# Kernel optimization log

Measured on AMD Instinct MI355X. Metric: run time of the kernel, lower is better.

Reference implementation:

```python
import jax, jax.numpy as jnp
import numpy as np

NCE_T = 0.07   # opt.nce_T
EPS = 1e-8     # torch CosineSimilarity eps
DIAG_FILL = -10.0

N, D = 8192, 256

def setup_inputs() -> dict:
    key = jax.random.key(0)
    kq, kk = jax.random.split(key)
    feat_q = jax.random.normal(kq, (N, D), dtype=jnp.float32)
    feat_k = jax.random.normal(kk, (N, D), dtype=jnp.float32)
    return {"feat_q": feat_q, "feat_k": feat_k}

def reference(feat_q, feat_k):
    # feat_k is detached in the original
    feat_k = jax.lax.stop_gradient(feat_k)
    nq = jnp.linalg.norm(feat_q, axis=-1)            # [N]
    nk = jnp.linalg.norm(feat_k, axis=-1)            # [N]
    # positive cosine similarity (paired rows)
    l_pos = jnp.sum(feat_q * feat_k, axis=-1) / jnp.maximum(nq * nk, EPS)  # [N]
    # full N x N cosine similarity via GEMM (torch does a broadcasted version)
    sim = (feat_q @ feat_k.T) / jnp.maximum(nq[:, None] * nk[None, :], EPS)  # [N,N]
    # mask self-similarities with -10.0 BEFORE dividing by temperature
    diag = jnp.eye(sim.shape[0], dtype=bool)
    l_neg = jnp.where(diag, DIAG_FILL, sim)
    out = jnp.concatenate([l_pos[:, None], l_neg], axis=1) / NCE_T  # [N, N+1]
    # cross-entropy vs target class 0, reduction='none'
    loss = jax.scipy.special.logsumexp(out, axis=1) - out[:, 0]     # [N]
    return loss
```

## Files before the change

### kernel.cpp

```cpp
#include <hip/hip_runtime.h>
#include <stdint.h>
#include <math.h>

#define NROWS 8192
#define DDIM  256
#define BM    128
#define GJ    8
#define COLS_PER_GROUP (NROWS / GJ)

constexpr float INV_T  = 1.0f / 0.07f;
constexpr float LOG2E  = 1.44269504f;
constexpr float K1     = INV_T * LOG2E;

typedef __bf16 bf16x8 __attribute__((ext_vector_type(8)));
typedef float  f32x4  __attribute__((ext_vector_type(4)));

__device__ __forceinline__ void async_copy16(const uint16_t* g, uint16_t* l) {
    __builtin_amdgcn_global_load_lds(
        (const __attribute__((address_space(1))) uint32_t*)g,
        (__attribute__((address_space(3))) uint32_t*)l, 16, 0, 0);
}

__device__ inline uint16_t f2bf(float f) {
    uint32_t u = __float_as_uint(f);
    u += 0x7fffu + ((u >> 16) & 1u);
    return (uint16_t)(u >> 16);
}

__global__ __launch_bounds__(256) void norm_lpos_kernel(
    const float* __restrict__ fq, const float* __restrict__ fk,
    uint16_t* __restrict__ qb, uint16_t* __restrict__ kb,
    float* __restrict__ lpT)
{
    const int wave = threadIdx.x >> 6;
    const int lane = threadIdx.x & 63;
    const int row  = blockIdx.x * 4 + wave;

    float4 vq = ((const float4*)(fq + (size_t)row * DDIM))[lane];
    float4 vk = ((const float4*)(fk + (size_t)row * DDIM))[lane];
    float sq = vq.x*vq.x + vq.y*vq.y + vq.z*vq.z + vq.w*vq.w;
    float sk = vk.x*vk.x + vk.y*vk.y + vk.z*vk.z + vk.w*vk.w;
    float dp = vq.x*vk.x + vq.y*vk.y + vq.z*vk.z + vq.w*vk.w;
    #pragma unroll
    for (int m = 1; m < 64; m <<= 1) {
        sq += __shfl_xor(sq, m, 64);
        sk += __shfl_xor(sk, m, 64);
        dp += __shfl_xor(dp, m, 64);
    }
    float rq = rsqrtf(sq), rk = rsqrtf(sk);

    ushort4 oq, ok;
    oq.x = f2bf(vq.x * rq); oq.y = f2bf(vq.y * rq); oq.z = f2bf(vq.z * rq); oq.w = f2bf(vq.w * rq);
    ok.x = f2bf(vk.x * rk); ok.y = f2bf(vk.y * rk); ok.z = f2bf(vk.z * rk); ok.w = f2bf(vk.w * rk);
    ((ushort4*)(qb + (size_t)row * DDIM))[lane] = oq;
    ((ushort4*)(kb + (size_t)row * DDIM))[lane] = ok;
    if (lane == 0) lpT[row] = dp * rq * rk * INV_T;
}

__global__ __launch_bounds__(256, 2) void nce_main_kernel(
    const uint16_t* __restrict__ qb, const uint16_t* __restrict__ kb,
    float* __restrict__ gpl)
{
    __shared__ __align__(16) uint16_t lds[2 * 128 * 128];

    const int tid    = threadIdx.x;
    const int wave   = tid >> 6;
    const int lane   = tid & 63;
    const int quad   = lane >> 4;
    const int lanelo = lane & 15;
    const int wr     = wave >> 1;
    const int wc     = wave & 1;
    const int rowBase      = blockIdx.x * BM;
    const int colGroupBase = blockIdx.y * COLS_PER_GROUP;

    #pragma unroll
    for (int i = 0; i < 16; ++i) {
        int S   = (wave * 16 + i) * 64 + lane;
        int row = S >> 5;
        int ch  = (S & 31) ^ (row & 31);
        async_copy16(qb + (size_t)(rowBase + row) * DDIM + ch * 8,
                     lds + (size_t)(wave * 16 + i) * 512);
    }
    __syncthreads();

    bf16x8 aq[4][8];
    #pragma unroll
    for (int mt = 0; mt < 4; ++mt) {
        int rq  = wr * 64 + mt * 16 + lanelo;
        int r31 = rq & 31;
        #pragma unroll
        for (int kk = 0; kk < 8; ++kk)
            aq[mt][kk] = *(const bf16x8*)&lds[rq * 256 + (((kk << 2) + quad) ^ r31) * 8];
    }
    __syncthreads();

    int koff[8];
    #pragma unroll
    for (int i = 0; i < 8; ++i) {
        int S   = i * 256 + tid;
        int row = S >> 4;
        int ch  = (S & 15) ^ (row & 15);
        koff[i] = (colGroupBase + row) * DDIM + ch * 8;
    }

    #pragma unroll
    for (int i = 0; i < 8; ++i)
        async_copy16(kb + koff[i], lds + (i * 256 + wave * 64) * 8);
    __syncthreads();

    int bvrow[4];
    #pragma unroll
    for (int nt = 0; nt < 4; ++nt) bvrow[nt] = (wc * 64 + nt * 16 + lanelo) * 128;

    float l_run[16];
    #pragma unroll
    for (int i = 0; i < 16; ++i) l_run[i] = 0.f;

    for (int jt = 0; jt < 8; ++jt) {
        f32x4 acc[4][4];
        #pragma unroll
        for (int mt = 0; mt < 4; ++mt)
            #pragma unroll
            for (int nt = 0; nt < 4; ++nt)
                acc[mt][nt] = (f32x4){0.f, 0.f, 0.f, 0.f};

        #pragma unroll
        for (int h = 0; h < 2; ++h) {
            const int p    = jt * 2 + h;
            const int buf  = p & 1;
            const int boff = buf << 14;

            if (p < 15) {
                const int np  = p + 1;
                const int soff = ((np >> 1) << 15) + ((np & 1) << 7);
                const int doff = (buf ^ 1) << 14;
                #pragma unroll
                for (int i = 0; i < 8; ++i)
                    async_copy16(kb + koff[i] + soff,
                                 lds + doff + (i * 256 + wave * 64) * 8);
            }

            #pragma unroll
            for (int kc = 0; kc < 4; ++kc) {
                bf16x8 bv[4];
                #pragma unroll
                for (int nt = 0; nt < 4; ++nt)
                    bv[nt] = *(const bf16x8*)&lds[boff + bvrow[nt] + (((kc << 2) + quad) ^ lanelo) * 8];
                #pragma unroll
                for (int mt = 0; mt < 4; ++mt)
                    #pragma unroll
                    for (int nt = 0; nt < 4; ++nt)
                        acc[mt][nt] = __builtin_amdgcn_mfma_f32_16x16x32_bf16(
                            aq[mt][h * 4 + kc], bv[nt], acc[mt][nt], 0, 0, 0);
            }
            __syncthreads();
        }

        #pragma unroll
        for (int mt = 0; mt < 4; ++mt)
            #pragma unroll
            for (int rg = 0; rg < 4; ++rg) {
                float s = 0.f;
                #pragma unroll
                for (int nt = 0; nt < 4; ++nt)
                    s += exp2f(fmaf(acc[mt][nt][rg], K1, -K1));
                l_run[mt * 4 + rg] += s;
            }
    }

    #pragma unroll
    for (int i = 0; i < 16; ++i) {
        float v = l_run[i];
        v += __shfl_xor(v, 1, 64);
        v += __shfl_xor(v, 2, 64);
        v += __shfl_xor(v, 4, 64);
        v += __shfl_xor(v, 8, 64);
        l_run[i] = v;
    }
    float* pl = (float*)lds;
    if (lanelo == 0) {
        #pragma unroll
        for (int mt = 0; mt < 4; ++mt)
            #pragma unroll
            for (int rg = 0; rg < 4; ++rg) {
                int lr = wr * 64 + mt * 16 + quad * 4 + rg;
                pl[wc * 128 + lr] = l_run[mt * 4 + rg];
            }
    }
    __syncthreads();
    if (tid < 128) {
        float L = pl[tid] + pl[128 + tid];
        gpl[(size_t)blockIdx.y * NROWS + rowBase + tid] = L;
    }
}

__global__ __launch_bounds__(256) void finalize_kernel(
    const float* __restrict__ gpl, const float* __restrict__ lpT,
    float* __restrict__ out)
{
    int t = blockIdx.x * 256 + threadIdx.x;
    if (t >= NROWS) return;
    float L = 0.f;
    #pragma unroll
    for (int g = 0; g < GJ; ++g) L += gpl[g * NROWS + t];
    out[t] = INV_T + __logf(L) - lpT[t];
}

extern "C" void kernel_launch(void* const* d_in, const int* in_sizes, int n_in,
                              void* d_out, int out_size, void* d_ws, size_t ws_size,
                              hipStream_t stream) {
    const float* fq = (const float*)d_in[0];
    const float* fk = (const float*)d_in[1];
    char* ws = (char*)d_ws;
    uint16_t* qb  = (uint16_t*)(ws);
    uint16_t* kb  = (uint16_t*)(ws + 4194304);
    float*    lpT = (float*)(ws + 8388608);
    float*    gpl = (float*)(ws + 8421376);

    norm_lpos_kernel<<<NROWS / 4, 256, 0, stream>>>(fq, fk, qb, kb, lpT);
    dim3 grid(NROWS / BM, GJ);
    nce_main_kernel<<<grid, 256, 0, stream>>>(qb, kb, gpl);
    finalize_kernel<<<NROWS / 256, 256, 0, stream>>>(gpl, lpT, (float*)d_out);
}
```

Measured before the change: 113.7 us.

## Stream Q and K tiles in 32-wide K-chunks instead of caching Q in registers

```diff
diff --git a/kernel.cpp b/kernel.cpp
--- a/kernel.cpp
+++ b/kernel.cpp
@@ -5,7 +5,8 @@
 #define NROWS 8192
 #define DDIM  256
 #define BM    128
-#define GJ    8
+#define BN    128
+#define GJ    16
 #define COLS_PER_GROUP (NROWS / GJ)
 
 constexpr float INV_T  = 1.0f / 0.07f;
@@ -57,11 +58,11 @@
     if (lane == 0) lpT[row] = dp * rq * rk * INV_T;
 }
 
-__global__ __launch_bounds__(256, 2) void nce_main_kernel(
+__global__ __launch_bounds__(256) void nce_main_kernel(
     const uint16_t* __restrict__ qb, const uint16_t* __restrict__ kb,
     float* __restrict__ gpl)
 {
-    __shared__ __align__(16) uint16_t lds[2 * 128 * 128];
+    __shared__ __align__(16) uint16_t lds[2][2][128 * 32];
 
     const int tid    = threadIdx.x;
     const int wave   = tid >> 6;
@@ -73,50 +74,40 @@
     const int rowBase      = blockIdx.x * BM;
     const int colGroupBase = blockIdx.y * COLS_PER_GROUP;
 
-    #pragma unroll
-    for (int i = 0; i < 16; ++i) {
-        int S   = (wave * 16 + i) * 64 + lane;
-        int row = S >> 5;
-        int ch  = (S & 31) ^ (row & 31);
-        async_copy16(qb + (size_t)(rowBase + row) * DDIM + ch * 8,
-                     lds + (size_t)(wave * 16 + i) * 512);
+    const uint16_t* qsrc[2];
+    const uint16_t* ksrc[2];
+    int dstoff[2];
+    #pragma unroll
+    for (int i = 0; i < 2; ++i) {
+        int S   = i * 256 + tid;
+        int row = S >> 2, cp = S & 3;
+        int cg  = ((cp + (row >> 2)) & 3) ^ (row & 3);
+        qsrc[i] = qb + (size_t)(rowBase + row) * DDIM + cg * 8;
+        ksrc[i] = kb + (size_t)(colGroupBase + row) * DDIM + cg * 8;
+        dstoff[i] = (i * 256 + wave * 64) * 8;
+    }
+
+    int avoff[4], bvoff[4];
+    #pragma unroll
+    for (int t = 0; t < 4; ++t) {
+        int ra = wr * 64 + t * 16 + lanelo;
+        avoff[t] = ra * 32 + ((((quad ^ (ra & 3)) - (ra >> 2)) & 3) * 8);
+        int rb = wc * 64 + t * 16 + lanelo;
+        bvoff[t] = rb * 32 + ((((quad ^ (rb & 3)) - (rb >> 2)) & 3) * 8);
+    }
+
+    #pragma unroll
+    for (int i = 0; i < 2; ++i) {
+        async_copy16(qsrc[i], &lds[0][0][0] + dstoff[i]);
+        async_copy16(ksrc[i], &lds[0][1][0] + dstoff[i]);
     }
     __syncthreads();
 
-    bf16x8 aq[4][8];
-    #pragma unroll
-    for (int mt = 0; mt < 4; ++mt) {
-        int rq  = wr * 64 + mt * 16 + lanelo;
-        int r31 = rq & 31;
-        #pragma unroll
-        for (int kk = 0; kk < 8; ++kk)
-            aq[mt][kk] = *(const bf16x8*)&lds[rq * 256 + (((kk << 2) + quad) ^ r31) * 8];
-    }
-    __syncthreads();
-
-    int koff[8];
-    #pragma unroll
-    for (int i = 0; i < 8; ++i) {
-        int S   = i * 256 + tid;
-        int row = S >> 4;
-        int ch  = (S & 15) ^ (row & 15);
-        koff[i] = (colGroupBase + row) * DDIM + ch * 8;
-    }
-
-    #pragma unroll
-    for (int i = 0; i < 8; ++i)
-        async_copy16(kb + koff[i], lds + (i * 256 + wave * 64) * 8);
-    __syncthreads();
-
-    int bvrow[4];
-    #pragma unroll
-    for (int nt = 0; nt < 4; ++nt) bvrow[nt] = (wc * 64 + nt * 16 + lanelo) * 128;
-
     float l_run[16];
     #pragma unroll
     for (int i = 0; i < 16; ++i) l_run[i] = 0.f;
 
-    for (int jt = 0; jt < 8; ++jt) {
+    for (int jt = 0; jt < COLS_PER_GROUP / BN; ++jt) {
         f32x4 acc[4][4];
         #pragma unroll
         for (int mt = 0; mt < 4; ++mt)
@@ -125,34 +116,34 @@
                 acc[mt][nt] = (f32x4){0.f, 0.f, 0.f, 0.f};
 
         #pragma unroll
-        for (int h = 0; h < 2; ++h) {
-            const int p    = jt * 2 + h;
-            const int buf  = p & 1;
-            const int boff = buf << 14;
-
-            if (p < 15) {
-                const int np  = p + 1;
-                const int soff = ((np >> 1) << 15) + ((np & 1) << 7);
-                const int doff = (buf ^ 1) << 14;
+        for (int kk = 0; kk < 8; ++kk) {
+            const int p   = jt * 8 + kk;
+            const int buf = p & 1;
+
+            if (p < 31) {
+                const int np = p + 1;
+                const int qo = (np & 7) << 5;
+                const int ko = ((np >> 3) << 15) + ((np & 7) << 5);
                 #pragma unroll
-                for (int i = 0; i < 8; ++i)
-                    async_copy16(kb + koff[i] + soff,
-                                 lds + doff + (i * 256 + wave * 64) * 8);
+                for (int i = 0; i < 2; ++i) {
+                    async_copy16(qsrc[i] + qo, &lds[buf ^ 1][0][0] + dstoff[i]);
+                    async_copy16(ksrc[i] + ko, &lds[buf ^ 1][1][0] + dstoff[i]);
+                }
             }
 
-            #pragma unroll
-            for (int kc = 0; kc < 4; ++kc) {
-                bf16x8 bv[4];
+            bf16x8 av[4], bv[4];
+            #pragma unroll
+            for (int mt = 0; mt < 4; ++mt)
+                av[mt] = *(const bf16x8*)&lds[buf][0][avoff[mt]];
+            #pragma unroll
+            for (int nt = 0; nt < 4; ++nt)
+                bv[nt] = *(const bf16x8*)&lds[buf][1][bvoff[nt]];
+            #pragma unroll
+            for (int mt = 0; mt < 4; ++mt)
                 #pragma unroll
                 for (int nt = 0; nt < 4; ++nt)
-                    bv[nt] = *(const bf16x8*)&lds[boff + bvrow[nt] + (((kc << 2) + quad) ^ lanelo) * 8];
-                #pragma unroll
-                for (int mt = 0; mt < 4; ++mt)
-                    #pragma unroll
-                    for (int nt = 0; nt < 4; ++nt)
-                        acc[mt][nt] = __builtin_amdgcn_mfma_f32_16x16x32_bf16(
-                            aq[mt][h * 4 + kc], bv[nt], acc[mt][nt], 0, 0, 0);
-            }
+                    acc[mt][nt] = __builtin_amdgcn_mfma_f32_16x16x32_bf16(av[mt], bv[nt], acc[mt][nt], 0, 0, 0);
+
             __syncthreads();
         }
 
@@ -177,7 +168,7 @@
         v += __shfl_xor(v, 8, 64);
         l_run[i] = v;
     }
-    float* pl = (float*)lds;
+    float* pl = (float*)&lds[0][0][0];
     if (lanelo == 0) {
         #pragma unroll
         for (int mt = 0; mt < 4; ++mt)
```

Result: no change. 114.8 us (+1.0%).
